# Kernel tuning notes

Measured on AMD Instinct MI355X. Metric: run time of the kernel, lower is better.

Reference implementation:

```python
import jax, jax.numpy as jnp
import numpy as np

N_NODES = 20000
N_EDGES = 320000
T = 4
H = 128


def setup_inputs() -> dict:
    key = jax.random.key(0)
    k = jax.random.split(key, 8)
    nf = jax.random.normal(k[0], (N_NODES, T, H), dtype=jnp.float32)
    input_events = jax.random.randint(k[1], (N_NODES, T), 0, 2, dtype=jnp.int32)
    src = jax.random.randint(k[2], (N_EDGES,), 0, N_NODES, dtype=jnp.int32)
    dst = jax.random.randint(k[3], (N_EDGES,), 0, N_NODES, dtype=jnp.int32)
    # attention params (GAT-style additive attention, decomposed a = [a_src; a_dst])
    a_src = jax.random.normal(k[4], (H,), dtype=jnp.float32) / np.sqrt(H)
    a_dst = jax.random.normal(k[5], (H,), dtype=jnp.float32) / np.sqrt(H)
    # node model: Linear(2*h_dim -> h_dim) + ReLU (mpnn built with 2*h_dim input)
    W = jax.random.normal(k[6], (2 * H, H), dtype=jnp.float32) / np.sqrt(2 * H)
    b = jnp.zeros((H,), dtype=jnp.float32)
    return {"nf": nf, "input_events": input_events, "src": src, "dst": dst,
            "a_src": a_src, "a_dst": a_dst, "W": W, "b": b}


def reference(nf, input_events, src, dst, a_src, a_dst, W, b):
    # Vectorized over all T timesteps at once. An edge participates at timestep t
    # iff input_events[src_node, t] == 1 (this replaces the per-node nonzero loop).
    N = nf.shape[0]
    neg_inf = jnp.asarray(-1e9, nf.dtype)

    # per-node attention projections: [N, T]
    proj_s = jnp.einsum("nth,h->nt", nf, a_src)
    proj_d = jnp.einsum("nth,h->nt", nf, a_dst)

    logits = jax.nn.leaky_relu(proj_s[src] + proj_d[dst], 0.2)   # [E, T]
    active = input_events[src] == 1                               # [E, T]
    logits = jnp.where(active, logits, neg_inf)

    # masked segment softmax over incoming active edges of each dst node
    m = jax.ops.segment_max(logits, dst, num_segments=N)          # [N, T]
    ex = jnp.where(active, jnp.exp(logits - m[dst]), 0.0)         # [E, T]
    den = jax.ops.segment_sum(ex, dst, num_segments=N)            # [N, T]
    alpha = ex / jnp.maximum(den[dst], 1e-9)                      # [E, T]

    # aggregate attention-weighted source features: [N, T, H]
    msgs = alpha[..., None] * nf[src]                             # [E, T, H]
    agg = jax.ops.segment_sum(msgs, dst, num_segments=N)          # [N, T, H]

    # node update on concat([nf, agg]) -> 2*h_dim input, ReLU
    out = jax.nn.relu(jnp.concatenate([nf, agg], axis=-1) @ W + b)
    return out
```

## Files before the change

### kernel.cpp

```cpp
#include <hip/hip_runtime.h>
#include <hip/hip_bf16.h>
#include <math.h>

#define NN 20000
#define NE 320000
#define TT 4
#define HH 128
#define NT4 (NN * TT)
#define CAP 128

typedef __attribute__((ext_vector_type(8))) short short8v;
typedef __attribute__((ext_vector_type(4))) float f32x4;

static __device__ __forceinline__ unsigned short f2bf(float v) {
    union { float f; unsigned u; } x; x.f = v;
    unsigned r = x.u + 0x7fff + ((x.u >> 16) & 1);
    return (unsigned short)(r >> 16);
}
static __device__ __forceinline__ unsigned pack2bf(float a, float b) {
    return (unsigned)f2bf(a) | ((unsigned)f2bf(b) << 16);
}
static __device__ __forceinline__ float bf_lo(unsigned v) { return __uint_as_float(v << 16); }
static __device__ __forceinline__ float bf_hi(unsigned v) { return __uint_as_float(v & 0xffff0000u); }


__global__ __launch_bounds__(256) void fusedA_kernel(
        const float* __restrict__ nf, const int* __restrict__ events,
        const float* __restrict__ a_src, const float* __restrict__ a_dst,
        const float* __restrict__ W,
        float* __restrict__ psm, float* __restrict__ pdv,
        unsigned* __restrict__ nfbt, int* __restrict__ cnt,
        uint4* __restrict__ wp) {
    int blk = blockIdx.x, tid = threadIdx.x;
    if (blk < 2500) {
        int g = tid >> 4, l16 = tid & 15;
        int rowA = blk * 32 + g;
        int rowB = rowA + 16;
        const float4* nf4 = (const float4*)nf;
        float4 va0 = nf4[(size_t)rowA * 32 + l16 * 2];
        float4 va1 = nf4[(size_t)rowA * 32 + l16 * 2 + 1];
        float4 vb0 = nf4[(size_t)rowB * 32 + l16 * 2];
        float4 vb1 = nf4[(size_t)rowB * 32 + l16 * 2 + 1];
        float4 s0 = ((const float4*)a_src)[l16 * 2];
        float4 s1 = ((const float4*)a_src)[l16 * 2 + 1];
        float4 d0 = ((const float4*)a_dst)[l16 * 2];
        float4 d1 = ((const float4*)a_dst)[l16 * 2 + 1];

        float sA = va0.x*s0.x + va0.y*s0.y + va0.z*s0.z + va0.w*s0.w
                 + va1.x*s1.x + va1.y*s1.y + va1.z*s1.z + va1.w*s1.w;
        float dA = va0.x*d0.x + va0.y*d0.y + va0.z*d0.z + va0.w*d0.w
                 + va1.x*d1.x + va1.y*d1.y + va1.z*d1.z + va1.w*d1.w;
        float sB = vb0.x*s0.x + vb0.y*s0.y + vb0.z*s0.z + vb0.w*s0.w
                 + vb1.x*s1.x + vb1.y*s1.y + vb1.z*s1.z + vb1.w*s1.w;
        float dB = vb0.x*d0.x + vb0.y*d0.y + vb0.z*d0.z + vb0.w*d0.w
                 + vb1.x*d1.x + vb1.y*d1.y + vb1.z*d1.z + vb1.w*d1.w;

        int nA = rowA >> 2, tA = rowA & 3;
        int nB = rowB >> 2;
        uint4 qa;
        qa.x = pack2bf(va0.x, va0.y); qa.y = pack2bf(va0.z, va0.w);
        qa.z = pack2bf(va1.x, va1.y); qa.w = pack2bf(va1.z, va1.w);
        ((uint4*)nfbt)[((size_t)tA * NN + nA) * 16 + l16] = qa;
        uint4 qb;
        qb.x = pack2bf(vb0.x, vb0.y); qb.y = pack2bf(vb0.z, vb0.w);
        qb.z = pack2bf(vb1.x, vb1.y); qb.w = pack2bf(vb1.z, vb1.w);
        ((uint4*)nfbt)[((size_t)tA * NN + nB) * 16 + l16] = qb;

        #pragma unroll
        for (int o = 1; o < 16; o <<= 1) {
            sA += __shfl_xor(sA, o); dA += __shfl_xor(dA, o);
            sB += __shfl_xor(sB, o); dB += __shfl_xor(dB, o);
        }
        if (l16 == 0) {
            psm[rowA] = (events[rowA] == 1) ? sA : -1e30f;
            pdv[rowA] = dA;
            psm[rowB] = (events[rowB] == 1) ? sB : -1e30f;
            pdv[rowB] = dB;
        }
    } else if (blk < 2516) {
        int f = (blk - 2500) * 256 + tid;
        int lane  = f & 63;
        int tile  = f >> 6;
        int kstep = tile >> 3, ntile = tile & 7;
        int k0 = kstep * 32 + (lane >> 4) * 8;
        int n  = ntile * 16 + (lane & 15);
        unsigned short h[8];
        #pragma unroll
        for (int j = 0; j < 8; ++j)
            h[j] = f2bf(W[(size_t)(k0 + j) * HH + n]);
        uint4 q;
        q.x = h[0] | ((unsigned)h[1] << 16);
        q.y = h[2] | ((unsigned)h[3] << 16);
        q.z = h[4] | ((unsigned)h[5] << 16);
        q.w = h[6] | ((unsigned)h[7] << 16);
        wp[f] = q;
    } else {
        int idx = (blk - 2516) * 256 + tid;
        #pragma unroll
        for (int k = 0; k < 4; ++k) {
            int j = idx * 4 + k;
            if (j < NN) cnt[j] = 0;
        }
    }
}

__global__ void scatterA_kernel(const int* __restrict__ src, const int* __restrict__ dst,
                                const float* __restrict__ psm, const float* __restrict__ pdv,
                                int* __restrict__ cnt, uint4* __restrict__ sexe, int n) {
    int e = blockIdx.x * blockDim.x + threadIdx.x;
    if (e >= n) return;
    int s = src[e], d = dst[e];
    float4 ps4 = *(const float4*)&psm[s * 4];
    bool any = (ps4.x > -1e29f) | (ps4.y > -1e29f) | (ps4.z > -1e29f) | (ps4.w > -1e29f);
    if (!any) return;
    int pos = atomicAdd(&cnt[d], 1);
    if (pos >= CAP) return;
    float4 pd4 = *(const float4*)&pdv[d * 4];
    float x0 = ps4.x + pd4.x; x0 = (x0 > 0.f) ? x0 : 0.2f * x0;
    float x1 = ps4.y + pd4.y; x1 = (x1 > 0.f) ? x1 : 0.2f * x1;
    float x2 = ps4.z + pd4.z; x2 = (x2 > 0.f) ? x2 : 0.2f * x2;
    float x3 = ps4.w + pd4.w; x3 = (x3 > 0.f) ? x3 : 0.2f * x3;
    float e0 = __expf(x0), e1 = __expf(x1), e2 = __expf(x2), e3 = __expf(x3);
    uint4 q;
    q.x = (unsigned)s;
    q.y = pack2bf(e0, e1);
    q.z = pack2bf(e2, e3);
    q.w = 0;
    sexe[(size_t)d * CAP + pos] = q;
}

__global__ __launch_bounds__(256) void aggoutA_kernel(
        const uint4* __restrict__ nfbt4, const int* __restrict__ cnt,
        const uint4* __restrict__ sexe, const uint4* __restrict__ wp,
        const float* __restrict__ b, float* __restrict__ out) {
    __shared__ uint4 xs[512];
    __shared__ uint4 led[4][64];
    int tid = threadIdx.x;
    int d0 = blockIdx.x * 4;

    {
        int row = tid >> 4, kc = tid & 15;
        int n = d0 + (row >> 2), t = row & 3;
        uint4 q = nfbt4[((size_t)t * NN + n) * 16 + kc];
        xs[(row * 32 + kc) ^ (row & 7)] = q;
    }

    int w = tid >> 6, lane = tid & 63;
    int g = lane >> 4, l16 = lane & 15;

    {
        int d = d0 + w;
        int cd = cnt[d]; if (cd > CAP) cd = CAP;
        size_t off = (size_t)d * CAP;
        const uint4* nft = nfbt4 + (size_t)g * NN * 16;
        float a0=0.f,a1=0.f,a2=0.f,a3=0.f,a4=0.f,a5=0.f,a6=0.f,a7=0.f;
        float den = 0.f;
        for (int base = 0; base < cd; base += 64) {
            int i = base + lane;
            if (i < cd) led[w][lane] = sexe[off + i];
            int cnt2 = min(64, cd - base);
            int j = 0;
            for (; j + 4 <= cnt2; j += 4) {
                #pragma unroll
                for (int u = 0; u < 4; ++u) {
                    uint4 q = led[w][j + u];
                    unsigned packed = (g & 2) ? q.z : q.y;
                    float ex = (g & 1) ? bf_hi(packed) : bf_lo(packed);
                    den += ex;
                    if (ex > 0.f) {
                        uint4 v = nft[(size_t)q.x * 16 + l16];
                        a0 += ex * bf_lo(v.x); a1 += ex * bf_hi(v.x);
                        a2 += ex * bf_lo(v.y); a3 += ex * bf_hi(v.y);
                        a4 += ex * bf_lo(v.z); a5 += ex * bf_hi(v.z);
                        a6 += ex * bf_lo(v.w); a7 += ex * bf_hi(v.w);
                    }
                }
            }
            for (; j < cnt2; ++j) {
                uint4 q = led[w][j];
                unsigned packed = (g & 2) ? q.z : q.y;
                float ex = (g & 1) ? bf_hi(packed) : bf_lo(packed);
                den += ex;
                if (ex > 0.f) {
                    uint4 v = nft[(size_t)q.x * 16 + l16];
                    a0 += ex * bf_lo(v.x); a1 += ex * bf_hi(v.x);
                    a2 += ex * bf_lo(v.y); a3 += ex * bf_hi(v.y);
                    a4 += ex * bf_lo(v.z); a5 += ex * bf_hi(v.z);
                    a6 += ex * bf_lo(v.w); a7 += ex * bf_hi(v.w);
                }
            }
        }
        float scale = (den > 0.f) ? (1.f / den) : 0.f;
        int lrow = w * 4 + g;
        uint4 o;
        o.x = pack2bf(a0 * scale, a1 * scale);
        o.y = pack2bf(a2 * scale, a3 * scale);
        o.z = pack2bf(a4 * scale, a5 * scale);
        o.w = pack2bf(a6 * scale, a7 * scale);
        xs[(lrow * 32 + 16 + l16) ^ (lrow & 7)] = o;
    }
    __syncthreads();

    f32x4 acc0 = (f32x4){0.f, 0.f, 0.f, 0.f};
    f32x4 acc1 = (f32x4){0.f, 0.f, 0.f, 0.f};
    int arow = lane & 15;
    int nt0 = 2 * w, nt1 = 2 * w + 1;
    const uint4* wplane = wp + lane;
    #pragma unroll
    for (int ks = 0; ks < 8; ++ks) {
        int kc = ks * 4 + (lane >> 4);
        uint4 av = xs[(arow * 32 + kc) ^ (arow & 7)];
        short8v af = __builtin_bit_cast(short8v, av);
        uint4 bv0 = wplane[(ks * 8 + nt0) * 64];
        uint4 bv1 = wplane[(ks * 8 + nt1) * 64];
        short8v bf0 = __builtin_bit_cast(short8v, bv0);
        short8v bf1 = __builtin_bit_cast(short8v, bv1);
        acc0 = __builtin_amdgcn_mfma_f32_16x16x32_bf16(bf0, af, acc0, 0, 0, 0);
        acc1 = __builtin_amdgcn_mfma_f32_16x16x32_bf16(bf1, af, acc1, 0, 0, 0);
    }

    int col = lane & 15;
    int oq  = (lane >> 4) * 4;
    size_t orow = ((size_t)blockIdx.x * 16 + col) * HH;
    {
        float4 bv4 = *(const float4*)&b[nt0 * 16 + oq];
        float4 res;
        res.x = fmaxf(acc0[0] + bv4.x, 0.f);
        res.y = fmaxf(acc0[1] + bv4.y, 0.f);
        res.z = fmaxf(acc0[2] + bv4.z, 0.f);
        res.w = fmaxf(acc0[3] + bv4.w, 0.f);
        *(float4*)&out[orow + nt0 * 16 + oq] = res;
    }
    {
        float4 bv4 = *(const float4*)&b[nt1 * 16 + oq];
        float4 res;
        res.x = fmaxf(acc1[0] + bv4.x, 0.f);
        res.y = fmaxf(acc1[1] + bv4.y, 0.f);
        res.z = fmaxf(acc1[2] + bv4.z, 0.f);
        res.w = fmaxf(acc1[3] + bv4.w, 0.f);
        *(float4*)&out[orow + nt1 * 16 + oq] = res;
    }
}

__global__ void projB_kernel(const float* __restrict__ nf,
                             const int* __restrict__ events,
                             const float* __restrict__ a_src,
                             const float* __restrict__ a_dst,
                             float* __restrict__ psm, float* __restrict__ pdv,
                             int total) {
    int wid  = (blockIdx.x * blockDim.x + threadIdx.x) >> 6;
    int lane = threadIdx.x & 63;
    if (wid >= total) return;
    float2 v  = ((const float2*)nf)[(size_t)wid * 64 + lane];
    float2 as = ((const float2*)a_src)[lane];
    float2 ad = ((const float2*)a_dst)[lane];
    float s  = v.x * as.x + v.y * as.y;
    float dd = v.x * ad.x + v.y * ad.y;
    #pragma unroll
    for (int o = 32; o >= 1; o >>= 1) {
        s  += __shfl_xor(s, o);
        dd += __shfl_xor(dd, o);
    }
    if (lane == 0) {
        psm[wid] = (events[wid] == 1) ? s : -1e30f;
        pdv[wid] = dd;
    }
}

__global__ void histB_kernel(const int* __restrict__ dst, int* __restrict__ deg, int n) {
    int e = blockIdx.x * blockDim.x + threadIdx.x;
    if (e < n) atomicAdd(&deg[dst[e]], 1);
}

__global__ __launch_bounds__(1024) void scan1_kernel(
        const int* __restrict__ deg, int* __restrict__ offsets,
        int* __restrict__ bsum, int n) {
    __shared__ int wsum[16];
    int tid = threadIdx.x, lane = tid & 63, wid = tid >> 6;
    int i = blockIdx.x * 1024 + tid;
    int v = (i < n) ? deg[i] : 0;
    int inc = v;
    #pragma unroll
    for (int o = 1; o < 64; o <<= 1) {
        int x = __shfl_up(inc, o);
        if (lane >= o) inc += x;
    }
    if (lane == 63) wsum[wid] = inc;
    __syncthreads();
    if (wid == 0 && lane < 16) {
        int t = wsum[lane];
        int w2 = t;
        #pragma unroll
        for (int o = 1; o < 16; o <<= 1) {
            int x = __shfl_up(w2, o);
            if (lane >= o) w2 += x;
        }
        wsum[lane] = w2 - t;
    }
    __syncthreads();
    int incl = wsum[wid] + inc;
    if (i < n) offsets[i + 1] = incl;
    if (tid == 1023) bsum[blockIdx.x] = incl;
}

__global__ __launch_bounds__(1024) void scan2_kernel(
        const int* __restrict__ bsum, int* __restrict__ offsets,
        int* __restrict__ cursor, int n) {
    __shared__ int base_s;
    int tid = threadIdx.x, blk = blockIdx.x;
    if (tid < 64) {
        int s = 0;
        for (int j = tid; j < blk; j += 64) s += bsum[j];
        #pragma unroll
        for (int o = 32; o >= 1; o >>= 1) s += __shfl_xor(s, o);
        if (tid == 0) base_s = s;
    }
    __syncthreads();
    int i = blk * 1024 + tid;
    if (i < n) {
        int v = offsets[i + 1] + base_s;
        offsets[i + 1] = v;
        cursor[i + 1]  = v;
    }
    if (blk == 0 && tid == 0) { offsets[0] = 0; cursor[0] = 0; }
}

__global__ void scatterB_kernel(const int* __restrict__ src, const int* __restrict__ dst,
                                int* __restrict__ cursor, int* __restrict__ ssrc, int n) {
    int e = blockIdx.x * blockDim.x + threadIdx.x;
    if (e < n) {
        int pos = atomicAdd(&cursor[dst[e]], 1);
        ssrc[pos] = src[e];
    }
}

__global__ __launch_bounds__(256) void aggB_kernel(
        const float* __restrict__ nf,
        const float* __restrict__ psm,
        const float* __restrict__ pdv,
        const int* __restrict__ offsets,
        const int* __restrict__ ssrc,
        float* __restrict__ agg) {
    __shared__ int2 led[TT][64];
    int t    = threadIdx.x >> 6;
    int lane = threadIdx.x & 63;
    int d    = blockIdx.x;
    int off = offsets[d], end = offsets[d + 1];
    float pd = pdv[d * TT + t];
    const float2* nf2 = (const float2*)nf;
    size_t tl = (size_t)t * 64 + lane;

    float2 acc = {0.f, 0.f};
    float den = 0.f;
    for (int base = off; base < end; base += 64) {
        int i = base + lane;
        float ex = 0.f; int s = 0;
        if (i < end) {
            s = ssrc[i];
            float p = psm[s * TT + t];
            if (p > -1e29f) {
                float x = p + pd;
                x = (x > 0.f) ? x : 0.2f * x;
                ex = __expf(x);
            }
        }
        den += ex;
        unsigned long long mask = __ballot(ex > 0.f);
        int nact = __popcll(mask);
        if (ex > 0.f) {
            int pos = __popcll(mask & ((1ull << lane) - 1ull));
            led[t][pos] = make_int2(s, __float_as_int(ex));
        }
        int j = 0;
        for (; j + 4 <= nact; j += 4) {
            int2 a0 = led[t][j], a1 = led[t][j + 1], a2 = led[t][j + 2], a3 = led[t][j + 3];
            float2 r0 = nf2[(size_t)a0.x * 256 + tl];
            float2 r1 = nf2[(size_t)a1.x * 256 + tl];
            float2 r2 = nf2[(size_t)a2.x * 256 + tl];
            float2 r3 = nf2[(size_t)a3.x * 256 + tl];
            float e0 = __int_as_float(a0.y), e1 = __int_as_float(a1.y);
            float e2 = __int_as_float(a2.y), e3 = __int_as_float(a3.y);
            acc.x += e0 * r0.x; acc.y += e0 * r0.y;
            acc.x += e1 * r1.x; acc.y += e1 * r1.y;
            acc.x += e2 * r2.x; acc.y += e2 * r2.y;
            acc.x += e3 * r3.x; acc.y += e3 * r3.y;
        }
        for (; j < nact; ++j) {
            int2 a = led[t][j];
            float2 r = nf2[(size_t)a.x * 256 + tl];
            float e = __int_as_float(a.y);
            acc.x += e * r.x; acc.y += e * r.y;
        }
    }
    #pragma unroll
    for (int o = 32; o >= 1; o >>= 1) den += __shfl_xor(den, o);
    float scale = (den > 0.f) ? (1.f / den) : 0.f;
    float2 res; res.x = acc.x * scale; res.y = acc.y * scale;
    ((float2*)agg)[(size_t)d * 256 + tl] = res;
}

__global__ void wpackB_kernel(const float* __restrict__ W, uint4* __restrict__ wp) {
    int f = blockIdx.x * blockDim.x + threadIdx.x;
    if (f >= 8 * 8 * 64) return;
    int lane  = f & 63;
    int tile  = f >> 6;
    int kstep = tile >> 3, ntile = tile & 7;
    int k0 = kstep * 32 + (lane >> 4) * 8;
    int n  = ntile * 16 + (lane & 15);
    unsigned short h[8];
    #pragma unroll
    for (int j = 0; j < 8; ++j)
        h[j] = f2bf(W[(size_t)(k0 + j) * HH + n]);
    uint4 q;
    q.x = h[0] | ((unsigned)h[1] << 16);
    q.y = h[2] | ((unsigned)h[3] << 16);
    q.z = h[4] | ((unsigned)h[5] << 16);
    q.w = h[6] | ((unsigned)h[7] << 16);
    wp[f] = q;
}

__global__ __launch_bounds__(256) void outB_kernel(
        const float* __restrict__ nf, const uint4* __restrict__ wp,
        const float* __restrict__ b, float* __restrict__ out) {
    __shared__ uint4 xs[2048];
    int tid = threadIdx.x;
    size_t row0 = (size_t)blockIdx.x * 64;

    #pragma unroll
    for (int i = 0; i < 8; ++i) {
        int c = i * 256 + tid;
        int row = c >> 5, kc = c & 31;
        const float* srcp = (kc < 16) ? (nf  + (row0 + row) * HH + kc * 8)
                                      : (out + (row0 + row) * HH + (kc - 16) * 8);
        float4 v0 = *reinterpret_cast<const float4*>(srcp);
        float4 v1 = *reinterpret_cast<const float4*>(srcp + 4);
        uint4 q;
        q.x = pack2bf(v0.x, v0.y);
        q.y = pack2bf(v0.z, v0.w);
        q.z = pack2bf(v1.x, v1.y);
        q.w = pack2bf(v1.z, v1.w);
        xs[(row * 32 + kc) ^ (row & 7)] = q;
    }
    __syncthreads();

    int w = tid >> 6, l = tid & 63;
    f32x4 acc[8];
    #pragma unroll
    for (int nt = 0; nt < 8; ++nt) acc[nt] = (f32x4){0.f, 0.f, 0.f, 0.f};

    int arow = w * 16 + (l & 15);
    const uint4* wplane = wp + l;
    #pragma unroll
    for (int ks = 0; ks < 8; ++ks) {
        int kc = ks * 4 + (l >> 4);
        uint4 av = xs[(arow * 32 + kc) ^ (arow & 7)];
        short8v af = __builtin_bit_cast(short8v, av);
        #pragma unroll
        for (int nt = 0; nt < 8; ++nt) {
            uint4 bv = wplane[(ks * 8 + nt) * 64];
            short8v bf = __builtin_bit_cast(short8v, bv);
            acc[nt] = __builtin_amdgcn_mfma_f32_16x16x32_bf16(bf, af, acc[nt], 0, 0, 0);
        }
    }

    int col = l & 15;
    int oq  = (l >> 4) * 4;
    size_t orow = (row0 + w * 16 + col) * HH;
    #pragma unroll
    for (int nt = 0; nt < 8; ++nt) {
        float4 bv4 = *(const float4*)&b[nt * 16 + oq];
        float4 res;
        res.x = fmaxf(acc[nt][0] + bv4.x, 0.f);
        res.y = fmaxf(acc[nt][1] + bv4.y, 0.f);
        res.z = fmaxf(acc[nt][2] + bv4.z, 0.f);
        res.w = fmaxf(acc[nt][3] + bv4.w, 0.f);
        *(float4*)&out[orow + nt * 16 + oq] = res;
    }
}

extern "C" void kernel_launch(void* const* d_in, const int* in_sizes, int n_in,
                              void* d_out, int out_size, void* d_ws, size_t ws_size,
                              hipStream_t stream) {
    const float* nf      = (const float*)d_in[0];
    const int*   events  = (const int*)  d_in[1];
    const int*   src     = (const int*)  d_in[2];
    const int*   dst     = (const int*)  d_in[3];
    const float* a_src   = (const float*)d_in[4];
    const float* a_dst   = (const float*)d_in[5];
    const float* W       = (const float*)d_in[6];
    const float* b       = (const float*)d_in[7];
    float* out = (float*)d_out;

    const int total_nt = NT4;
    char* ws = (char*)d_ws;

    const size_t NEED_A = 21265664;
    if (ws_size >= NEED_A) {
        unsigned* nfbt  = (unsigned*)(ws);
        float* psm      = (float*)(ws + 20480000);
        float* pdv      = (float*)(ws + 20800000);
        int*   cnt      = (int*)  (ws + 21120000);
        uint4* wpack    = (uint4*)(ws + 21200128);
        uint4* sexe     = (uint4*)d_out;

        fusedA_kernel<<<2536, 256, 0, stream>>>(nf, events, a_src, a_dst, W,
                                                psm, pdv, nfbt, cnt, wpack);
        scatterA_kernel<<<(NE + 255) / 256, 256, 0, stream>>>(src, dst, psm, pdv,
                                                              cnt, sexe, NE);
        aggoutA_kernel<<<NN / 4, 256, 0, stream>>>((const uint4*)nfbt, cnt, sexe,
                                                   wpack, b, out);
    } else {
        float* psm     = (float*)(ws);
        float* pdv     = (float*)(ws + 1310720);
        int*   offsets = (int*)  (ws + 2621440);
        int*   deg     = (int*)  (ws + 2703360);
        int*   cursor  = (int*)  (ws + 2785280);
        int*   ssrc    = (int*)  (ws + 2867200);
        uint4* wpack   = (uint4*)(ws);
        int*   bsumB   = (int*)  (ws + 4147200);

        const int SCAN_B = (NN + 1023) / 1024;
        hipMemsetAsync(deg, 0, NN * sizeof(int), stream);
        projB_kernel<<<total_nt / 4, 256, 0, stream>>>(nf, events, a_src, a_dst, psm, pdv, total_nt);
        histB_kernel<<<(NE + 255) / 256, 256, 0, stream>>>(dst, deg, NE);
        scan1_kernel<<<SCAN_B, 1024, 0, stream>>>(deg, offsets, bsumB, NN);
        scan2_kernel<<<SCAN_B, 1024, 0, stream>>>(bsumB, offsets, cursor, NN);
        scatterB_kernel<<<(NE + 255) / 256, 256, 0, stream>>>(src, dst, cursor, ssrc, NE);
        aggB_kernel<<<NN, 256, 0, stream>>>(nf, psm, pdv, offsets, ssrc, out);
        wpackB_kernel<<<16, 256, 0, stream>>>(W, wpack);
        outB_kernel<<<total_nt / 64, 256, 0, stream>>>(nf, wpack, b, out);
    }
}
```

Baseline: 81.48 us.

## Sort destination nodes by in-degree to balance warps in aggregation kernel

Adds a single-block counting-sort kernel that orders destination nodes by their clamped active-edge count, then has the aggregation/output kernel process nodes in that order so the four warps in each block handle nodes of similar degree. Output rows are written to the permuted node's location. This targets load imbalance between warps sharing a block, at the cost of an extra serial one-block launch and scattered feature/output accesses.

```diff
diff --git a/kernel.cpp b/kernel.cpp
--- a/kernel.cpp
+++ b/kernel.cpp
@@ -8,6 +8,7 @@
 #define HH 128
 #define NT4 (NN * TT)
 #define CAP 128
+#define NBUCK (CAP + 1)
 
 typedef __attribute__((ext_vector_type(8))) short short8v;
 typedef __attribute__((ext_vector_type(4))) float f32x4;
@@ -129,28 +130,70 @@
     sexe[(size_t)d * CAP + pos] = q;
 }
 
+__global__ __launch_bounds__(1024) void sortd_kernel(
+        const int* __restrict__ cnt, int* __restrict__ dorder) {
+    __shared__ int hist[16][NBUCK];
+    __shared__ int boff[NBUCK];
+    int tid = threadIdx.x, wid = tid >> 6;
+    for (int i = tid; i < 16 * NBUCK; i += 1024) ((int*)hist)[i] = 0;
+    __syncthreads();
+    int cdv[20];
+    #pragma unroll
+    for (int k = 0; k < 20; ++k) {
+        int d = k * 1024 + tid;
+        int c = (d < NN) ? min(cnt[d], CAP) : -1;
+        cdv[k] = c;
+        if (c >= 0) atomicAdd(&hist[wid][c], 1);
+    }
+    __syncthreads();
+    if (tid < NBUCK) {
+        int tot = 0;
+        #pragma unroll
+        for (int w2 = 0; w2 < 16; ++w2) tot += hist[w2][tid];
+        boff[tid] = tot;
+    }
+    __syncthreads();
+    if (tid == 0) {
+        int run = 0;
+        for (int bkt = 0; bkt < NBUCK; ++bkt) {
+            int t = boff[bkt]; boff[bkt] = run; run += t;
+        }
+    }
+    __syncthreads();
+    #pragma unroll
+    for (int k = 0; k < 20; ++k) {
+        int c = cdv[k];
+        if (c >= 0) {
+            int pos = atomicAdd(&boff[c], 1);
+            dorder[pos] = k * 1024 + tid;
+        }
+    }
+}
+
 __global__ __launch_bounds__(256) void aggoutA_kernel(
         const uint4* __restrict__ nfbt4, const int* __restrict__ cnt,
+        const int* __restrict__ dorder,
         const uint4* __restrict__ sexe, const uint4* __restrict__ wp,
         const float* __restrict__ b, float* __restrict__ out) {
     __shared__ uint4 xs[512];
     __shared__ uint4 led[4][64];
     int tid = threadIdx.x;
-    int d0 = blockIdx.x * 4;
+    int4 dd = *(const int4*)&dorder[blockIdx.x * 4];
+    int w = tid >> 6, lane = tid & 63;
+    int g = lane >> 4, l16 = lane & 15;
+
+    int d = (w == 0) ? dd.x : (w == 1) ? dd.y : (w == 2) ? dd.z : dd.w;
+    int cd = cnt[d]; if (cd > CAP) cd = CAP;
 
     {
         int row = tid >> 4, kc = tid & 15;
-        int n = d0 + (row >> 2), t = row & 3;
+        int di = row >> 2, t = row & 3;
+        int n = (di == 0) ? dd.x : (di == 1) ? dd.y : (di == 2) ? dd.z : dd.w;
         uint4 q = nfbt4[((size_t)t * NN + n) * 16 + kc];
         xs[(row * 32 + kc) ^ (row & 7)] = q;
     }
 
-    int w = tid >> 6, lane = tid & 63;
-    int g = lane >> 4, l16 = lane & 15;
-
     {
-        int d = d0 + w;
-        int cd = cnt[d]; if (cd > CAP) cd = CAP;
         size_t off = (size_t)d * CAP;
         const uint4* nft = nfbt4 + (size_t)g * NN * 16;
         float a0=0.f,a1=0.f,a2=0.f,a3=0.f,a4=0.f,a5=0.f,a6=0.f,a7=0.f;
@@ -221,7 +264,9 @@
 
     int col = lane & 15;
     int oq  = (lane >> 4) * 4;
-    size_t orow = ((size_t)blockIdx.x * 16 + col) * HH;
+    int dic = col >> 2, tc = col & 3;
+    int dcol = (dic == 0) ? dd.x : (dic == 1) ? dd.y : (dic == 2) ? dd.z : dd.w;
+    size_t orow = ((size_t)dcol * 4 + tc) * HH;
     {
         float4 bv4 = *(const float4*)&b[nt0 * 16 + oq];
         float4 res;
@@ -494,21 +539,23 @@
     const int total_nt = NT4;
     char* ws = (char*)d_ws;
 
-    const size_t NEED_A = 21265664;
+    const size_t NEED_A = 21345664;
     if (ws_size >= NEED_A) {
         unsigned* nfbt  = (unsigned*)(ws);
         float* psm      = (float*)(ws + 20480000);
         float* pdv      = (float*)(ws + 20800000);
         int*   cnt      = (int*)  (ws + 21120000);
         uint4* wpack    = (uint4*)(ws + 21200128);
+        int*   dorder   = (int*)  (ws + 21265664);
         uint4* sexe     = (uint4*)d_out;
 
         fusedA_kernel<<<2536, 256, 0, stream>>>(nf, events, a_src, a_dst, W,
                                                 psm, pdv, nfbt, cnt, wpack);
         scatterA_kernel<<<(NE + 255) / 256, 256, 0, stream>>>(src, dst, psm, pdv,
                                                               cnt, sexe, NE);
-        aggoutA_kernel<<<NN / 4, 256, 0, stream>>>((const uint4*)nfbt, cnt, sexe,
-                                                   wpack, b, out);
+        sortd_kernel<<<1, 1024, 0, stream>>>(cnt, dorder);
+        aggoutA_kernel<<<NN / 4, 256, 0, stream>>>((const uint4*)nfbt, cnt, dorder,
+                                                   sexe, wpack, b, out);
     } else {
         float* psm     = (float*)(ws);
         float* pdv     = (float*)(ws + 1310720);
```

Result: slower. 93.54 us (+14.8%).

## Split each destination's edge list across two waves and reduce partials in LDS

Applied to the files above, without the earlier changes.

The aggregation kernel now runs 512 threads per block, with two wavefronts per destination node, each handling half of its incoming edge list. Partial accumulators and denominators go to shared memory and are combined before the bf16 pack. The MFMA output stage is spread over 8 waves with one 16-column tile each instead of two. This is meant to raise parallelism and memory-level concurrency for the latency-bound gather. The cost is more shared memory (about 18KB of partials), an extra barrier and reduction step, and possibly lower occupancy per CU.

```diff
diff --git a/kernel.cpp b/kernel.cpp
--- a/kernel.cpp
+++ b/kernel.cpp
@@ -129,36 +129,43 @@
     sexe[(size_t)d * CAP + pos] = q;
 }
 
-__global__ __launch_bounds__(256) void aggoutA_kernel(
+__global__ __launch_bounds__(512) void aggoutA_kernel(
         const uint4* __restrict__ nfbt4, const int* __restrict__ cnt,
         const uint4* __restrict__ sexe, const uint4* __restrict__ wp,
         const float* __restrict__ b, float* __restrict__ out) {
     __shared__ uint4 xs[512];
-    __shared__ uint4 led[4][64];
+    __shared__ uint4 led[8][64];
+    __shared__ float part[8][64][9];
+    __shared__ float dsh[8][4];
     int tid = threadIdx.x;
     int d0 = blockIdx.x * 4;
-
-    {
+    int w = tid >> 6, lane = tid & 63;
+    int g = lane >> 4, l16 = lane & 15;
+
+    int di = w >> 1, half = w & 1;
+    int d = d0 + di;
+    int cd = cnt[d]; if (cd > CAP) cd = CAP;
+    int h1 = (cd + 1) >> 1;
+    int lo = half ? h1 : 0;
+    int hi = half ? cd : h1;
+    int myn = hi - lo;
+
+    if (tid < 256) {
         int row = tid >> 4, kc = tid & 15;
         int n = d0 + (row >> 2), t = row & 3;
         uint4 q = nfbt4[((size_t)t * NN + n) * 16 + kc];
         xs[(row * 32 + kc) ^ (row & 7)] = q;
     }
 
-    int w = tid >> 6, lane = tid & 63;
-    int g = lane >> 4, l16 = lane & 15;
-
     {
-        int d = d0 + w;
-        int cd = cnt[d]; if (cd > CAP) cd = CAP;
-        size_t off = (size_t)d * CAP;
+        size_t off = (size_t)d * CAP + lo;
         const uint4* nft = nfbt4 + (size_t)g * NN * 16;
         float a0=0.f,a1=0.f,a2=0.f,a3=0.f,a4=0.f,a5=0.f,a6=0.f,a7=0.f;
         float den = 0.f;
-        for (int base = 0; base < cd; base += 64) {
+        for (int base = 0; base < myn; base += 64) {
             int i = base + lane;
-            if (i < cd) led[w][lane] = sexe[off + i];
-            int cnt2 = min(64, cd - base);
+            if (i < myn) led[w][lane] = sexe[off + i];
+            int cnt2 = min(64, myn - base);
             int j = 0;
             for (; j + 4 <= cnt2; j += 4) {
                 #pragma unroll
@@ -190,56 +197,55 @@
                 }
             }
         }
+        float* p = part[w][lane];
+        p[0] = a0; p[1] = a1; p[2] = a2; p[3] = a3;
+        p[4] = a4; p[5] = a5; p[6] = a6; p[7] = a7;
+        if (l16 == 0) dsh[w][g] = den;
+    }
+    __syncthreads();
+
+    if (tid < 256) {
+        int lrow = tid >> 4, l16c = tid & 15;
+        int dic = lrow >> 2, gc = lrow & 3;
+        int wA = dic * 2, wB = wA + 1;
+        float den = dsh[wA][gc] + dsh[wB][gc];
         float scale = (den > 0.f) ? (1.f / den) : 0.f;
-        int lrow = w * 4 + g;
+        const float* pA = part[wA][gc * 16 + l16c];
+        const float* pB = part[wB][gc * 16 + l16c];
+        float r0 = (pA[0] + pB[0]) * scale, r1 = (pA[1] + pB[1]) * scale;
+        float r2 = (pA[2] + pB[2]) * scale, r3 = (pA[3] + pB[3]) * scale;
+        float r4 = (pA[4] + pB[4]) * scale, r5 = (pA[5] + pB[5]) * scale;
+        float r6 = (pA[6] + pB[6]) * scale, r7 = (pA[7] + pB[7]) * scale;
         uint4 o;
-        o.x = pack2bf(a0 * scale, a1 * scale);
-        o.y = pack2bf(a2 * scale, a3 * scale);
-        o.z = pack2bf(a4 * scale, a5 * scale);
-        o.w = pack2bf(a6 * scale, a7 * scale);
-        xs[(lrow * 32 + 16 + l16) ^ (lrow & 7)] = o;
+        o.x = pack2bf(r0, r1); o.y = pack2bf(r2, r3);
+        o.z = pack2bf(r4, r5); o.w = pack2bf(r6, r7);
+        xs[(lrow * 32 + 16 + l16c) ^ (lrow & 7)] = o;
     }
     __syncthreads();
 
-    f32x4 acc0 = (f32x4){0.f, 0.f, 0.f, 0.f};
-    f32x4 acc1 = (f32x4){0.f, 0.f, 0.f, 0.f};
+    f32x4 acc = (f32x4){0.f, 0.f, 0.f, 0.f};
     int arow = lane & 15;
-    int nt0 = 2 * w, nt1 = 2 * w + 1;
     const uint4* wplane = wp + lane;
     #pragma unroll
     for (int ks = 0; ks < 8; ++ks) {
         int kc = ks * 4 + (lane >> 4);
         uint4 av = xs[(arow * 32 + kc) ^ (arow & 7)];
         short8v af = __builtin_bit_cast(short8v, av);
-        uint4 bv0 = wplane[(ks * 8 + nt0) * 64];
-        uint4 bv1 = wplane[(ks * 8 + nt1) * 64];
-        short8v bf0 = __builtin_bit_cast(short8v, bv0);
-        short8v bf1 = __builtin_bit_cast(short8v, bv1);
-        acc0 = __builtin_amdgcn_mfma_f32_16x16x32_bf16(bf0, af, acc0, 0, 0, 0);
-        acc1 = __builtin_amdgcn_mfma_f32_16x16x32_bf16(bf1, af, acc1, 0, 0, 0);
+        uint4 bv = wplane[(ks * 8 + w) * 64];
+        short8v bf = __builtin_bit_cast(short8v, bv);
+        acc = __builtin_amdgcn_mfma_f32_16x16x32_bf16(bf, af, acc, 0, 0, 0);
     }
 
     int col = lane & 15;
     int oq  = (lane >> 4) * 4;
     size_t orow = ((size_t)blockIdx.x * 16 + col) * HH;
-    {
-        float4 bv4 = *(const float4*)&b[nt0 * 16 + oq];
-        float4 res;
-        res.x = fmaxf(acc0[0] + bv4.x, 0.f);
-        res.y = fmaxf(acc0[1] + bv4.y, 0.f);
-        res.z = fmaxf(acc0[2] + bv4.z, 0.f);
-        res.w = fmaxf(acc0[3] + bv4.w, 0.f);
-        *(float4*)&out[orow + nt0 * 16 + oq] = res;
-    }
-    {
-        float4 bv4 = *(const float4*)&b[nt1 * 16 + oq];
-        float4 res;
-        res.x = fmaxf(acc1[0] + bv4.x, 0.f);
-        res.y = fmaxf(acc1[1] + bv4.y, 0.f);
-        res.z = fmaxf(acc1[2] + bv4.z, 0.f);
-        res.w = fmaxf(acc1[3] + bv4.w, 0.f);
-        *(float4*)&out[orow + nt1 * 16 + oq] = res;
-    }
+    float4 bv4 = *(const float4*)&b[w * 16 + oq];
+    float4 res;
+    res.x = fmaxf(acc[0] + bv4.x, 0.f);
+    res.y = fmaxf(acc[1] + bv4.y, 0.f);
+    res.z = fmaxf(acc[2] + bv4.z, 0.f);
+    res.w = fmaxf(acc[3] + bv4.w, 0.f);
+    *(float4*)&out[orow + w * 16 + oq] = res;
 }
 
 __global__ void projB_kernel(const float* __restrict__ nf,
@@ -507,7 +513,7 @@
                                                 psm, pdv, nfbt, cnt, wpack);
         scatterA_kernel<<<(NE + 255) / 256, 256, 0, stream>>>(src, dst, psm, pdv,
                                                               cnt, sexe, NE);
-        aggoutA_kernel<<<NN / 4, 256, 0, stream>>>((const uint4*)nfbt, cnt, sexe,
+        aggoutA_kernel<<<NN / 4, 512, 0, stream>>>((const uint4*)nfbt, cnt, sexe,
                                                    wpack, b, out);
     } else {
         float* psm     = (float*)(ws);
```

After: 83.71 us. 2.7% more time.
